# Performance work log

Hardware: AMD Instinct MI355X
Metric: run time of the kernel (lower is better)

Reference implementation:

```python
import jax, jax.numpy as jnp
import numpy as np

DIM = 512
HEADS = 8
DIM_HEAD = 64
HIDDEN = HEADS * DIM_HEAD  # 512
SCALE = DIM_HEAD ** -0.5


def setup_inputs() -> dict:
    key = jax.random.key(0)
    k1, k2, k3 = jax.random.split(key, 3)
    x = jax.random.normal(k1, (4, 2048, DIM), dtype=jnp.float32)
    # torch Linear weight convention: [out_features, in_features], y = x @ W.T
    W_qkv = jax.random.normal(k2, (3 * HIDDEN, DIM), dtype=jnp.float32) * (DIM ** -0.5)
    W_out = jax.random.normal(k3, (DIM, HIDDEN), dtype=jnp.float32) * (HIDDEN ** -0.5)
    return {"x": x, "W_qkv": W_qkv, "W_out": W_out}


def reference(x, W_qkv, W_out):
    b, n, c = x.shape
    qkv = jnp.einsum('bnc,oc->bno', x, W_qkv)  # [b, n, 3*hidden]
    q, k, v = jnp.split(qkv, 3, axis=-1)
    # rearrange 'b n (h c) -> b h c n'
    def to_heads(t):
        return jnp.transpose(t.reshape(b, n, HEADS, DIM_HEAD), (0, 2, 3, 1))
    q, k, v = to_heads(q), to_heads(k), to_heads(v)
    q = q * SCALE
    sim = jnp.einsum('bhcn,bhcj->bhnj', q, k)  # [b, h, n, n]
    attn = jax.nn.softmax(sim, axis=-1)
    out = jnp.einsum('bhnj,bhdj->bhnd', attn, v)  # [b, h, n, d]
    out = jnp.transpose(out, (0, 2, 1, 3)).reshape(b, n, HIDDEN)  # 'b h n d -> b n (h d)'
    return jnp.einsum('bnh,oh->bno', out, W_out)
```

## Files before the change

### kernel.cpp

```cpp
#include <hip/hip_runtime.h>


typedef unsigned short u16;
typedef __attribute__((ext_vector_type(8))) short s16x8;
typedef __attribute__((ext_vector_type(4))) float f32x4;
typedef __attribute__((ext_vector_type(16))) float f32x16;

__device__ __forceinline__ u16 f2bf(float f) {
  unsigned int u = __float_as_uint(f);
  u = (u + 0x7fffu + ((u >> 16) & 1u)) >> 16;
  return (u16)u;
}

__device__ __forceinline__ void gload16(const u16* g, u16* lds_base) {
  __builtin_amdgcn_global_load_lds(
      (const __attribute__((address_space(1))) unsigned int*)g,
      (__attribute__((address_space(3))) unsigned int*)lds_base, 16, 0, 0);
}

__global__ __launch_bounds__(256) void cvt4(const float* __restrict__ in,
                                            u16* __restrict__ out, int n4) {
  int i = blockIdx.x * 256 + threadIdx.x;
  if (i >= n4) return;
  float4 f = ((const float4*)in)[i];
  uint2 o;
  o.x = (unsigned)f2bf(f.x) | ((unsigned)f2bf(f.y) << 16);
  o.y = (unsigned)f2bf(f.z) | ((unsigned)f2bf(f.w) << 16);
  ((uint2*)out)[i] = o;
}

template <int BN, int MODE>
__global__ __launch_bounds__(256) void gemm128(
    const u16* __restrict__ A, const u16* __restrict__ B,
    float* __restrict__ Cf,
    u16* __restrict__ Qp, u16* __restrict__ Kp, u16* __restrict__ Vp) {
  constexpr int K = 512;
  constexpr int JN = BN / 32;
  __shared__ u16 smem[128 * 64 + BN * 64];
  u16* As = smem;
  u16* Bs = smem + 128 * 64;
  const int bm0 = blockIdx.x * 128, bn0 = blockIdx.y * BN;
  const int t = threadIdx.x, wave = t >> 6, lane = t & 63;
  const int quad = lane >> 4, l16 = lane & 15;
  const int wm = (wave & 1) * 64, wn = (wave >> 1) * (BN / 2);
  const int lr = lane >> 3, lc = lane & 7;
  const int swz = lc ^ lr;

  f32x4 acc[4][JN] = {};

  for (int k0 = 0; k0 < K; k0 += 64) {
    __syncthreads();
#pragma unroll
    for (int a = 0; a < 4; a++) {
      int r = wave * 32 + a * 8 + lr;
      gload16(A + (size_t)(bm0 + r) * K + k0 + swz * 8,
              &As[(wave * 32 + a * 8) * 64]);
    }
#pragma unroll
    for (int b = 0; b < BN / 32; b++) {
      int r = wave * (BN / 4) + b * 8 + lr;
      gload16(B + (size_t)(bn0 + r) * K + k0 + swz * 8,
              &Bs[(wave * (BN / 4) + b * 8) * 64]);
    }
    __syncthreads();
#pragma unroll
    for (int ks = 0; ks < 2; ks++) {
      s16x8 af[4], bf[JN];
#pragma unroll
      for (int i = 0; i < 4; i++) {
        int m = wm + i * 16 + l16;
        af[i] = *(const s16x8*)(&As[m * 64 + (((ks * 4 + quad) ^ (m & 7)) * 8)]);
      }
#pragma unroll
      for (int j = 0; j < JN; j++) {
        int n = wn + j * 16 + l16;
        bf[j] = *(const s16x8*)(&Bs[n * 64 + (((ks * 4 + quad) ^ (n & 7)) * 8)]);
      }
#pragma unroll
      for (int i = 0; i < 4; i++)
#pragma unroll
        for (int j = 0; j < JN; j++)
          acc[i][j] = __builtin_amdgcn_mfma_f32_16x16x32_bf16(af[i], bf[j], acc[i][j], 0, 0, 0);
    }
  }

  if constexpr (MODE == 1) {
#pragma unroll
    for (int i = 0; i < 4; i++)
#pragma unroll
      for (int j = 0; j < JN; j++)
#pragma unroll
        for (int r = 0; r < 4; r++) {
          int m = bm0 + wm + i * 16 + quad * 4 + r;
          int n = bn0 + wn + j * 16 + l16;
          Cf[(size_t)m * 512 + n] = acc[i][j][r];
        }
  } else {
    const int part = bn0 >> 9;
    if (part < 2) {
#pragma unroll
      for (int i = 0; i < 4; i++)
#pragma unroll
        for (int j = 0; j < JN; j++)
#pragma unroll
          for (int r = 0; r < 4; r++) {
            int m = bm0 + wm + i * 16 + quad * 4 + r;
            int n = bn0 + wn + j * 16 + l16;
            int oin = n & 511;
            int head = oin >> 6, dh = oin & 63;
            int bb = m >> 11, tok = m & 2047;
            size_t idx = ((size_t)(bb * 8 + head) * 2048 + tok) * 64 + dh;
            if (part == 0)
              Qp[idx] = f2bf(acc[i][j][r] * 0.18033688011112042f);
            else
              Kp[idx] = f2bf(acc[i][j][r]);
          }
    } else {
      __syncthreads();
#pragma unroll
      for (int i = 0; i < 4; i++)
#pragma unroll
        for (int j = 0; j < JN; j++)
#pragma unroll
          for (int r = 0; r < 4; r++) {
            int row = wm + i * 16 + quad * 4 + r;
            int cn = wn + j * 16 + l16;
            smem[row * 128 + (cn ^ (row & 7))] = f2bf(acc[i][j][r]);
          }
      __syncthreads();
      const int bb = bm0 >> 11;
      const int tokbase = bm0 & 2047;
      const int headbase = (bn0 & 511) >> 6;
#pragma unroll
      for (int it = 0; it < 8; it++) {
        int cn = it * 16 + (t >> 4);
        int dh = cn & 63, head = headbase + (cn >> 6);
        int tok0 = (t & 15) * 8;
        s16x8 pk;
#pragma unroll
        for (int k = 0; k < 8; k++) {
          int row = tok0 + k;
          pk[k] = (short)smem[row * 128 + (cn ^ (row & 7))];
        }
        *(s16x8*)(&Vp[((size_t)(bb * 8 + head) * 64 + dh) * 2048 + tokbase + tok0]) = pk;
      }
    }
  }
}

__global__ __launch_bounds__(256) void attn_kernel(
    const u16* __restrict__ Qg, const u16* __restrict__ Kg,
    const u16* __restrict__ Vtg, u16* __restrict__ Og) {
  __shared__ u16 Qs[64][72];
  __shared__ u16 Ks[64][72];
  __shared__ u16 Vt[64][72];
  __shared__ u16 Ps[64][72];
  __shared__ float Ls[2][64];
  const int bh = blockIdx.y;
  const int q0 = blockIdx.x * 64;
  const u16* Qh = Qg + (size_t)bh * 2048 * 64;
  const u16* Kh = Kg + (size_t)bh * 2048 * 64;
  const u16* Vh = Vtg + (size_t)bh * 64 * 2048;
  const int t = threadIdx.x, lane = t & 63, wave = t >> 6;
  const int wq = wave & 1, wk = wave >> 1;
  const int l32 = lane & 31, half = lane >> 5;
  const int srow = t >> 2, scolb = (t & 3) * 8;

#pragma unroll
  for (int p = 0; p < 2; p++) {
    int col = scolb + p * 32;
    *(s16x8*)(&Qs[srow][col]) = *(const s16x8*)(Qh + (size_t)(q0 + srow) * 64 + col);
  }
  __syncthreads();
  s16x8 aq[4];
#pragma unroll
  for (int ks = 0; ks < 4; ks++)
    aq[ks] = *(const s16x8*)(&Qs[wq * 32 + l32][ks * 16 + half * 8]);

  f32x16 o = {};
  float l_part[16];
#pragma unroll
  for (int r = 0; r < 16; r++) l_part[r] = 0.f;

  for (int j0 = 0; j0 < 2048; j0 += 64) {
    __syncthreads();
#pragma unroll
    for (int p = 0; p < 2; p++) {
      int col = scolb + p * 32;
      *(s16x8*)(&Ks[srow][col]) = *(const s16x8*)(Kh + (size_t)(j0 + srow) * 64 + col);
      *(s16x8*)(&Vt[srow][col]) = *(const s16x8*)(Vh + (size_t)srow * 2048 + j0 + col);
    }
    __syncthreads();

    f32x16 s = {};
#pragma unroll
    for (int ks = 0; ks < 4; ks++) {
      s16x8 bk = *(const s16x8*)(&Ks[wk * 32 + l32][ks * 16 + half * 8]);
      s = __builtin_amdgcn_mfma_f32_32x32x16_bf16(aq[ks], bk, s, 0, 0, 0);
    }

#pragma unroll
    for (int r = 0; r < 16; r++) {
      float p = __builtin_amdgcn_exp2f(s[r]);
      unsigned u = __float_as_uint(p);
      l_part[r] += __uint_as_float(u & 0xffff0000u);
      int row = (r & 3) + 8 * (r >> 2) + 4 * half + wq * 32;
      Ps[row][wk * 32 + l32] = (u16)(u >> 16);
    }
    __syncthreads();

#pragma unroll
    for (int ks = 0; ks < 4; ks++) {
      s16x8 ap = *(const s16x8*)(&Ps[wq * 32 + l32][ks * 16 + half * 8]);
      s16x8 bv = *(const s16x8*)(&Vt[wk * 32 + l32][ks * 16 + half * 8]);
      o = __builtin_amdgcn_mfma_f32_32x32x16_bf16(ap, bv, o, 0, 0, 0);
    }
  }

#pragma unroll
  for (int r = 0; r < 16; r++) {
#pragma unroll
    for (int msk = 1; msk < 32; msk <<= 1)
      l_part[r] += __shfl_xor(l_part[r], msk, 64);
  }
  if (l32 == 0) {
#pragma unroll
    for (int r = 0; r < 16; r++) {
      int rowl = (r & 3) + 8 * (r >> 2) + 4 * half;
      Ls[wk][wq * 32 + rowl] = l_part[r];
    }
  }
  __syncthreads();

  const int bb = bh >> 3, h = bh & 7;
#pragma unroll
  for (int r = 0; r < 16; r++) {
    int rowl = (r & 3) + 8 * (r >> 2) + 4 * half;
    float l = Ls[0][wq * 32 + rowl] + Ls[1][wq * 32 + rowl];
    float val = o[r] * __builtin_amdgcn_rcpf(l);
    int row = q0 + wq * 32 + rowl;
    Og[((size_t)bb * 2048 + row) * 512 + h * 64 + wk * 32 + l32] = f2bf(val);
  }
}

extern "C" void kernel_launch(void* const* d_in, const int* in_sizes, int n_in,
                              void* d_out, int out_size, void* d_ws, size_t ws_size,
                              hipStream_t stream) {
  const float* x    = (const float*)d_in[0];
  const float* Wqkv = (const float*)d_in[1];
  const float* Wout = (const float*)d_in[2];
  float* y = (float*)d_out;

  char* ws = (char*)d_ws;
  size_t off = 0;
  auto alloc = [&](size_t bytes) {
    void* p = ws + off;
    off += (bytes + 255) & ~(size_t)255;
    return p;
  };
  u16* xb    = (u16*)alloc((size_t)8192 * 512 * 2);
  u16* wqkvb = (u16*)alloc((size_t)1536 * 512 * 2);
  u16* woutb = (u16*)alloc((size_t)512 * 512 * 2);
  u16* Qw    = (u16*)alloc((size_t)32 * 2048 * 64 * 2);
  u16* Kw    = (u16*)alloc((size_t)32 * 2048 * 64 * 2);
  u16* Vw    = (u16*)alloc((size_t)32 * 2048 * 64 * 2);
  u16* Ow    = (u16*)alloc((size_t)8192 * 512 * 2);
  if (off > ws_size) return;

  cvt4<<<4096, 256, 0, stream>>>(x, xb, 8192 * 512 / 4);
  cvt4<<<768, 256, 0, stream>>>(Wqkv, wqkvb, 1536 * 512 / 4);
  cvt4<<<256, 256, 0, stream>>>(Wout, woutb, 512 * 512 / 4);

  gemm128<128, 0><<<dim3(64, 12), 256, 0, stream>>>(xb, wqkvb, nullptr, Qw, Kw, Vw);
  attn_kernel<<<dim3(32, 32), 256, 0, stream>>>(Qw, Kw, Vw, Ow);
  gemm128<64, 1><<<dim3(64, 8), 256, 0, stream>>>(Ow, woutb, y, nullptr, nullptr, nullptr);
}
```

Measured before the change: 175.1 us.

## Keep softmax probabilities in registers via permlane swap and merge conversion kernels

The attention kernel now computes S transposed (K as the A operand, Q as B) so that exp'd probabilities can be repacked in registers with byte perms and v_permlane32_swap into the B operand of the PV MFMA. This drops the P tile round-trip through shared memory and one barrier per KV block. Each wave now splits the KV columns by wk and accumulates the full 64-wide output; the two partial outputs and row sums are reduced through LDS at the end, and the results are written as coalesced 16-byte stores. The three fp32-to-bf16 conversion launches are also merged into one kernel, saving launch overhead. The cost is twice the output accumulator registers and a final cross-wave reduction step.

```diff
diff --git a/kernel.cpp b/kernel.cpp
--- a/kernel.cpp
+++ b/kernel.cpp
@@ -18,15 +18,28 @@
       (__attribute__((address_space(3))) unsigned int*)lds_base, 16, 0, 0);
 }
 
-__global__ __launch_bounds__(256) void cvt4(const float* __restrict__ in,
-                                            u16* __restrict__ out, int n4) {
+__device__ __forceinline__ void permlane32_swap(unsigned& a, unsigned& b) {
+  asm volatile("v_permlane32_swap_b32 %0, %1" : "+v"(a), "+v"(b));
+}
+
+__global__ __launch_bounds__(256) void cvt_all(
+    const float* __restrict__ x, const float* __restrict__ w1,
+    const float* __restrict__ w2, u16* __restrict__ xb,
+    u16* __restrict__ w1b, u16* __restrict__ w2b) {
+  constexpr int N1 = 8192 * 512 / 4, N2 = 1536 * 512 / 4, N3 = 512 * 512 / 4;
   int i = blockIdx.x * 256 + threadIdx.x;
-  if (i >= n4) return;
-  float4 f = ((const float4*)in)[i];
+  if (i >= N1 + N2 + N3) return;
+  const float* src;
+  u16* dst;
+  int j;
+  if (i < N1) { src = x; dst = xb; j = i; }
+  else if (i < N1 + N2) { src = w1; dst = w1b; j = i - N1; }
+  else { src = w2; dst = w2b; j = i - N1 - N2; }
+  float4 f = ((const float4*)src)[j];
   uint2 o;
   o.x = (unsigned)f2bf(f.x) | ((unsigned)f2bf(f.y) << 16);
   o.y = (unsigned)f2bf(f.z) | ((unsigned)f2bf(f.w) << 16);
-  ((uint2*)out)[i] = o;
+  ((uint2*)dst)[j] = o;
 }
 
 template <int BN, int MODE>
@@ -151,11 +164,13 @@
 __global__ __launch_bounds__(256) void attn_kernel(
     const u16* __restrict__ Qg, const u16* __restrict__ Kg,
     const u16* __restrict__ Vtg, u16* __restrict__ Og) {
-  __shared__ u16 Qs[64][72];
-  __shared__ u16 Ks[64][72];
-  __shared__ u16 Vt[64][72];
-  __shared__ u16 Ps[64][72];
-  __shared__ float Ls[2][64];
+  __shared__ __attribute__((aligned(16))) u16 smem[3 * 64 * 72];
+  u16* Qs = smem;
+  u16* Ks = smem + 64 * 72;
+  u16* Vt = smem + 2 * 64 * 72;
+  float* Obuf = (float*)smem;
+  float* Lbuf = (float*)((char*)smem + 64 * 68 * 4);
+
   const int bh = blockIdx.y;
   const int q0 = blockIdx.x * 64;
   const u16* Qh = Qg + (size_t)bh * 2048 * 64;
@@ -165,81 +180,120 @@
   const int wq = wave & 1, wk = wave >> 1;
   const int l32 = lane & 31, half = lane >> 5;
   const int srow = t >> 2, scolb = (t & 3) * 8;
+  const int q = wq * 32 + l32;
 
 #pragma unroll
   for (int p = 0; p < 2; p++) {
     int col = scolb + p * 32;
-    *(s16x8*)(&Qs[srow][col]) = *(const s16x8*)(Qh + (size_t)(q0 + srow) * 64 + col);
+    *(s16x8*)(&Qs[srow * 72 + col]) = *(const s16x8*)(Qh + (size_t)(q0 + srow) * 64 + col);
   }
   __syncthreads();
-  s16x8 aq[4];
+  s16x8 bQ[4];
 #pragma unroll
   for (int ks = 0; ks < 4; ks++)
-    aq[ks] = *(const s16x8*)(&Qs[wq * 32 + l32][ks * 16 + half * 8]);
-
-  f32x16 o = {};
-  float l_part[16];
-#pragma unroll
-  for (int r = 0; r < 16; r++) l_part[r] = 0.f;
+    bQ[ks] = *(const s16x8*)(&Qs[q * 72 + ks * 16 + half * 8]);
+
+  f32x16 o[2] = {};
+  float l_acc = 0.f;
 
   for (int j0 = 0; j0 < 2048; j0 += 64) {
     __syncthreads();
 #pragma unroll
     for (int p = 0; p < 2; p++) {
       int col = scolb + p * 32;
-      *(s16x8*)(&Ks[srow][col]) = *(const s16x8*)(Kh + (size_t)(j0 + srow) * 64 + col);
-      *(s16x8*)(&Vt[srow][col]) = *(const s16x8*)(Vh + (size_t)srow * 2048 + j0 + col);
+      *(s16x8*)(&Ks[srow * 72 + col]) = *(const s16x8*)(Kh + (size_t)(j0 + srow) * 64 + col);
+      *(s16x8*)(&Vt[srow * 72 + col]) = *(const s16x8*)(Vh + (size_t)srow * 2048 + j0 + col);
     }
     __syncthreads();
 
     f32x16 s = {};
 #pragma unroll
     for (int ks = 0; ks < 4; ks++) {
-      s16x8 bk = *(const s16x8*)(&Ks[wk * 32 + l32][ks * 16 + half * 8]);
-      s = __builtin_amdgcn_mfma_f32_32x32x16_bf16(aq[ks], bk, s, 0, 0, 0);
-    }
-
+      s16x8 aK = *(const s16x8*)(&Ks[(wk * 32 + l32) * 72 + ks * 16 + half * 8]);
+      s = __builtin_amdgcn_mfma_f32_32x32x16_bf16(aK, bQ[ks], s, 0, 0, 0);
+    }
+
+    unsigned pu[16];
 #pragma unroll
     for (int r = 0; r < 16; r++) {
       float p = __builtin_amdgcn_exp2f(s[r]);
       unsigned u = __float_as_uint(p);
-      l_part[r] += __uint_as_float(u & 0xffff0000u);
-      int row = (r & 3) + 8 * (r >> 2) + 4 * half + wq * 32;
-      Ps[row][wk * 32 + l32] = (u16)(u >> 16);
-    }
-    __syncthreads();
-
-#pragma unroll
-    for (int ks = 0; ks < 4; ks++) {
-      s16x8 ap = *(const s16x8*)(&Ps[wq * 32 + l32][ks * 16 + half * 8]);
-      s16x8 bv = *(const s16x8*)(&Vt[wk * 32 + l32][ks * 16 + half * 8]);
-      o = __builtin_amdgcn_mfma_f32_32x32x16_bf16(ap, bv, o, 0, 0, 0);
-    }
-  }
-
-#pragma unroll
-  for (int r = 0; r < 16; r++) {
-#pragma unroll
-    for (int msk = 1; msk < 32; msk <<= 1)
-      l_part[r] += __shfl_xor(l_part[r], msk, 64);
-  }
-  if (l32 == 0) {
-#pragma unroll
-    for (int r = 0; r < 16; r++) {
-      int rowl = (r & 3) + 8 * (r >> 2) + 4 * half;
-      Ls[wk][wq * 32 + rowl] = l_part[r];
-    }
-  }
+      l_acc += __uint_as_float(u & 0xffff0000u);
+      pu[r] = u;
+    }
+    unsigned g[8];
+#pragma unroll
+    for (int v = 0; v < 8; v++)
+      g[v] = __builtin_amdgcn_perm(pu[2 * v + 1], pu[2 * v], 0x07060302u);
+    permlane32_swap(g[0], g[2]);
+    permlane32_swap(g[1], g[3]);
+    permlane32_swap(g[4], g[6]);
+    permlane32_swap(g[5], g[7]);
+    s16x8 bP[2];
+    ((unsigned*)&bP[0])[0] = g[0]; ((unsigned*)&bP[0])[1] = g[1];
+    ((unsigned*)&bP[0])[2] = g[2]; ((unsigned*)&bP[0])[3] = g[3];
+    ((unsigned*)&bP[1])[0] = g[4]; ((unsigned*)&bP[1])[1] = g[5];
+    ((unsigned*)&bP[1])[2] = g[6]; ((unsigned*)&bP[1])[3] = g[7];
+
+#pragma unroll
+    for (int dt = 0; dt < 2; dt++)
+#pragma unroll
+      for (int s2 = 0; s2 < 2; s2++) {
+        s16x8 aV = *(const s16x8*)(&Vt[(dt * 32 + l32) * 72 + wk * 32 + s2 * 16 + half * 8]);
+        o[dt] = __builtin_amdgcn_mfma_f32_32x32x16_bf16(aV, bP[s2], o[dt], 0, 0, 0);
+      }
+  }
+
   __syncthreads();
-
-  const int bb = bh >> 3, h = bh & 7;
-#pragma unroll
-  for (int r = 0; r < 16; r++) {
-    int rowl = (r & 3) + 8 * (r >> 2) + 4 * half;
-    float l = Ls[0][wq * 32 + rowl] + Ls[1][wq * 32 + rowl];
-    float val = o[r] * __builtin_amdgcn_rcpf(l);
-    int row = q0 + wq * 32 + rowl;
-    Og[((size_t)bb * 2048 + row) * 512 + h * 64 + wk * 32 + l32] = f2bf(val);
+  Lbuf[(wk * 2 + half) * 64 + q] = l_acc;
+  if (wk == 1) {
+#pragma unroll
+    for (int dt = 0; dt < 2; dt++)
+#pragma unroll
+      for (int gi = 0; gi < 4; gi++) {
+        int d0 = 8 * gi + 4 * half + 32 * dt;
+        float4 v = { o[dt][4 * gi + 0], o[dt][4 * gi + 1],
+                     o[dt][4 * gi + 2], o[dt][4 * gi + 3] };
+        *(float4*)(&Obuf[q * 68 + d0]) = v;
+      }
+  }
+  __syncthreads();
+  if (wk == 0) {
+    float l = Lbuf[0 * 64 + q] + Lbuf[1 * 64 + q] + Lbuf[2 * 64 + q] + Lbuf[3 * 64 + q];
+    float sc = __builtin_amdgcn_rcpf(l);
+#pragma unroll
+    for (int dt = 0; dt < 2; dt++)
+#pragma unroll
+      for (int gi = 0; gi < 4; gi++) {
+        int d0 = 8 * gi + 4 * half + 32 * dt;
+        float4 v = *(float4*)(&Obuf[q * 68 + d0]);
+        v.x = (v.x + o[dt][4 * gi + 0]) * sc;
+        v.y = (v.y + o[dt][4 * gi + 1]) * sc;
+        v.z = (v.z + o[dt][4 * gi + 2]) * sc;
+        v.w = (v.w + o[dt][4 * gi + 3]) * sc;
+        *(float4*)(&Obuf[q * 68 + d0]) = v;
+      }
+  }
+  __syncthreads();
+
+  {
+    const int bb = bh >> 3, h = bh & 7;
+    int qq = t >> 2, d0 = (t & 3) * 16;
+    float f[16];
+#pragma unroll
+    for (int c = 0; c < 4; c++) {
+      float4 v = *(float4*)(&Obuf[qq * 68 + d0 + 4 * c]);
+      f[4 * c + 0] = v.x; f[4 * c + 1] = v.y; f[4 * c + 2] = v.z; f[4 * c + 3] = v.w;
+    }
+    unsigned pk[8];
+#pragma unroll
+    for (int c = 0; c < 8; c++)
+      pk[c] = (unsigned)f2bf(f[2 * c]) | ((unsigned)f2bf(f[2 * c + 1]) << 16);
+    size_t base = ((size_t)bb * 2048 + q0 + qq) * 512 + h * 64 + d0;
+    uint4 s0 = { pk[0], pk[1], pk[2], pk[3] };
+    uint4 s1 = { pk[4], pk[5], pk[6], pk[7] };
+    *(uint4*)(&Og[base]) = s0;
+    *(uint4*)(&Og[base + 8]) = s1;
   }
 }
 
@@ -267,9 +321,7 @@
   u16* Ow    = (u16*)alloc((size_t)8192 * 512 * 2);
   if (off > ws_size) return;
 
-  cvt4<<<4096, 256, 0, stream>>>(x, xb, 8192 * 512 / 4);
-  cvt4<<<768, 256, 0, stream>>>(Wqkv, wqkvb, 1536 * 512 / 4);
-  cvt4<<<256, 256, 0, stream>>>(Wout, woutb, 512 * 512 / 4);
+  cvt_all<<<5120, 256, 0, stream>>>(x, Wqkv, Wout, xb, wqkvb, woutb);
 
   gemm128<128, 0><<<dim3(64, 12), 256, 0, stream>>>(xb, wqkvb, nullptr, Qw, Kw, Vw);
   attn_kernel<<<dim3(32, 32), 256, 0, stream>>>(Qw, Kw, Vw, Ow);
```

Measured after the change: 171.2 us. 1.02x faster.
